# Kernel tuning notes

Measured on AMD Instinct MI355X. Metric: run time of the kernel, lower is better.

## Reference

```python
import jax, jax.numpy as jnp
import numpy as np

S, B, NC = 16, 8, 5
D, H, DH = 256, 16, 16
PS, IMG = 7, 28
P = (IMG // PS) ** 2  # 16 patches
L = 2
PD = PS * PS * 1  # 49
EF, EFT = 4, 0.5
DFT = int(EFT * D)


def layernorm(x, g, b, eps=1e-5):
    m = x.mean(-1, keepdims=True)
    v = ((x - m) ** 2).mean(-1, keepdims=True)
    return (x - m) / jnp.sqrt(v + eps) * g + b


def patchify(x):
    # 's b c (h p1) (w p2) -> s b (h w) (p1 p2 c)'
    s, bb, c, hh, ww = x.shape
    h, w = hh // PS, ww // PS
    x = x.reshape(s, bb, c, h, PS, w, PS)
    x = x.transpose(0, 1, 3, 5, 4, 6, 2)
    return x.reshape(s, bb, h * w, PS * PS * c)


def srwm(x, Wy, Wq, Wk, wb, ln_g, ln_b):
    # Stateful self-referential weight matrix layer (Irie et al. 2022).
    # x: (S, Bn, h*dh); Wy/Wq/Wk: (h, dh, dh); wb: (h, 4, dh)
    s, bn, dim = x.shape
    h, dh = Wy.shape[0], Wy.shape[1]
    xs = x.reshape(s, bn, h, dh)
    bc = lambda W: jnp.broadcast_to(W[None], (bn,) + W.shape)

    def step(carry, xt):
        Wy, Wq, Wk, wb = carry
        y = jnp.einsum('bhij,bhj->bhi', Wy, xt)
        q = jnp.einsum('bhij,bhj->bhi', Wq, xt)
        k = jnp.einsum('bhij,bhj->bhi', Wk, xt)
        beta = jax.nn.sigmoid(jnp.einsum('bhcj,bhj->bhc', wb, xt))  # (Bn,h,4)
        qs = jax.nn.softmax(q, -1)
        ks = jax.nn.softmax(k, -1)
        # old values retrieved with k, target values generated with q
        vy_k = jnp.einsum('bhij,bhj->bhi', Wy, ks)
        vq_k = jnp.einsum('bhij,bhj->bhi', Wq, ks)
        vk_k = jnp.einsum('bhij,bhj->bhi', Wk, ks)
        vb_k = jnp.einsum('bhcj,bhj->bhc', wb, ks)
        vy_q = jax.nn.softmax(jnp.einsum('bhij,bhj->bhi', Wy, qs), -1)
        vq_q = jnp.einsum('bhij,bhj->bhi', Wq, qs)
        vk_q = jnp.einsum('bhij,bhj->bhi', Wk, qs)
        vb_q = jnp.einsum('bhcj,bhj->bhc', wb, qs)
        upd = lambda d, bt: bt[..., None, None] * d[..., None] * ks[..., None, :]
        Wy = Wy + upd(vy_q - vy_k, beta[..., 0])
        Wq = Wq + upd(vq_q - vq_k, beta[..., 1])
        Wk = Wk + upd(vk_q - vk_k, beta[..., 2])
        wb = wb + beta[..., 3, None, None] * (vb_q - vb_k)[..., None] * ks[..., None, :]
        return (Wy, Wq, Wk, wb), y

    _, ys = jax.lax.scan(step, (bc(Wy), bc(Wq), bc(Wk), bc(wb)), xs)
    return layernorm(ys.reshape(s, bn, dim), ln_g, ln_b)


def setup_inputs():
    key = jax.random.key(0)
    ks = iter(jax.random.split(key, 64))
    n = lambda shape, sc: jax.random.normal(next(ks), shape, jnp.float32) * sc
    return dict(
        x=jax.random.normal(next(ks), (S, B, 1, IMG, IMG), jnp.float32),
        fb=jax.random.randint(next(ks), (S, B), 0, NC),
        in_W=n((PD + NC, D), (PD + NC) ** -0.5), in_b=jnp.zeros((D,)),
        tk_Wy=n((L, 1, P, P), P ** -0.5), tk_Wq=n((L, 1, P, P), 0.01 * P ** -0.5),
        tk_Wk=n((L, 1, P, P), P ** -0.5), tk_wb=n((L, 1, 4, P), P ** -0.5),
        tk_lng=jnp.ones((L, P)), tk_lnb=jnp.zeros((L, P)),
        tkm_g=jnp.ones((L, D)), tkm_b=jnp.zeros((L, D)),
        tkm_W1=n((L, P, EF * P), P ** -0.5), tkm_b1=jnp.zeros((L, EF * P)),
        tkm_W2=n((L, EF * P, P), (EF * P) ** -0.5), tkm_b2=jnp.zeros((L, P)),
        ch_Wy=n((L, H, DH, DH), DH ** -0.5), ch_Wq=n((L, H, DH, DH), 0.01 * DH ** -0.5),
        ch_Wk=n((L, H, DH, DH), DH ** -0.5), ch_wb=n((L, H, 4, DH), DH ** -0.5),
        ch_lng=jnp.ones((L, D)), ch_lnb=jnp.zeros((L, D)),
        chm_g=jnp.ones((L, D)), chm_b=jnp.zeros((L, D)),
        chm_W1=n((L, D, DFT), D ** -0.5), chm_b1=jnp.zeros((L, DFT)),
        chm_W2=n((L, DFT, D), DFT ** -0.5), chm_b2=jnp.zeros((L, D)),
        fln_g=jnp.ones((D,)), fln_b=jnp.zeros((D,)),
        o_Wy=n((H, DH, DH), DH ** -0.5), o_Wq=n((H, DH, DH), 0.01 * DH ** -0.5),
        o_Wk=n((H, DH, DH), DH ** -0.5), o_wb=n((H, 4, DH), DH ** -0.5),
        o_lng=jnp.ones((D,)), o_lnb=jnp.zeros((D,)),
        out_W=n((D, NC), D ** -0.5), out_b=jnp.zeros((NC,)),
    )


def reference(x, fb, in_W, in_b, tk_Wy, tk_Wq, tk_Wk, tk_wb, tk_lng, tk_lnb,
              tkm_g, tkm_b, tkm_W1, tkm_b1, tkm_W2, tkm_b2,
              ch_Wy, ch_Wq, ch_Wk, ch_wb, ch_lng, ch_lnb,
              chm_g, chm_b, chm_W1, chm_b1, chm_W2, chm_b2,
              fln_g, fln_b, o_Wy, o_Wq, o_Wk, o_wb, o_lng, o_lnb, out_W, out_b):
    xp = patchify(x)  # (S,B,P,PD)
    emb = jnp.broadcast_to(jax.nn.one_hot(fb, NC)[:, :, None, :], (S, B, P, NC))
    h = jnp.concatenate([xp, emb.astype(xp.dtype)], -1) @ in_W + in_b  # (S,B,P,D)
    for i in range(L):
        # token SRWM: features = patch axis, batch = B*D
        t = jnp.swapaxes(h, -2, -1).reshape(S, B * D, P)
        t = srwm(t, tk_Wy[i], tk_Wq[i], tk_Wk[i], tk_wb[i], tk_lng[i], tk_lnb[i])
        h = jnp.swapaxes(t.reshape(S, B, D, P), -2, -1)
        # token mixer (pre-norm residual, FFN over patch axis)
        hn = jnp.swapaxes(layernorm(h, tkm_g[i], tkm_b[i]), -2, -1)
        hn = jax.nn.gelu(hn @ tkm_W1[i] + tkm_b1[i]) @ tkm_W2[i] + tkm_b2[i]
        h = h + jnp.swapaxes(hn, -2, -1)
        # channel SRWM: features = hidden axis, batch = B*P
        c = srwm(h.reshape(S, B * P, D), ch_Wy[i], ch_Wq[i], ch_Wk[i], ch_wb[i], ch_lng[i], ch_lnb[i])
        h = c.reshape(S, B, P, D)
        # channel mixer
        hn = layernorm(h, chm_g[i], chm_b[i])
        h = h + (jax.nn.gelu(hn @ chm_W1[i] + chm_b1[i]) @ chm_W2[i] + chm_b2[i])
    h = layernorm(h, fln_g, fln_b).mean(-2)  # (S,B,D) mean over patches
    h = srwm(h, o_Wy, o_Wq, o_Wk, o_wb, o_lng, o_lnb)
    return h @ out_W + out_b  # (S,B,NC)
```

## Files before the change

### kernel.cpp

```cpp
#include <hip/hip_runtime.h>
#include <math.h>

constexpr int cS  = 16;
constexpr int cB  = 8;
constexpr int cNC = 5;
constexpr int cD  = 256;
constexpr int cP  = 16;
constexpr int cPD = 49;
#define LEPS 1e-5f

__device__ __forceinline__ float frcp(float x) { return __builtin_amdgcn_rcpf(x); }
__device__ __forceinline__ float sigm(float x) { return frcp(1.0f + __expf(-x)); }
__device__ __forceinline__ float gelu_t(float x) {
  const float z = 1.5957691216057308f * (x + 0.044715f * x * x * x);
  return x * frcp(1.0f + __expf(-z));
}

template<int CTRL>
__device__ __forceinline__ float dpp_mov(float v) {
  return __int_as_float(__builtin_amdgcn_update_dpp(
      0, __float_as_int(v), CTRL, 0xF, 0xF, true));
}
__device__ __forceinline__ float row_sum16(float v) {
  v += dpp_mov<0xB1>(v);
  v += dpp_mov<0x4E>(v);
  v += dpp_mov<0x124>(v);
  v += dpp_mov<0x128>(v);
  return v;
}
__device__ __forceinline__ float wave_sum64(float v) {
  v = row_sum16(v);
  v += __shfl_xor(v, 16, 64);
  v += __shfl_xor(v, 32, 64);
  return v;
}

__global__ __launch_bounds__(256) void k_embed(const float* __restrict__ x,
                                               const int* __restrict__ fb,
                                               const float* __restrict__ inW,
                                               const float* __restrict__ inb,
                                               float* __restrict__ h) {
  const int blk = blockIdx.x;
  const int p  = blk & 15;
  const int sb = blk >> 4;
  const int ph = p >> 2, pw = p & 3;
  __shared__ float sx[cPD];
  const int t = threadIdx.x;
  if (t < cPD) {
    const int p1 = t / 7, p2 = t % 7;
    sx[t] = x[(size_t)sb * 784 + (ph * 7 + p1) * 28 + (pw * 7 + p2)];
  }
  __syncthreads();
  const int cls = fb[sb];
  float acc = inb[t] + inW[(size_t)(cPD + cls) * cD + t];
#pragma unroll
  for (int j = 0; j < cPD; ++j) acc += sx[j] * inW[(size_t)j * cD + t];
  h[((size_t)sb * cP + p) * cD + t] = acc;
}

__global__ __launch_bounds__(256) void k_tok_srwm(
    float* __restrict__ h, const float* __restrict__ Wy0, const float* __restrict__ Wq0,
    const float* __restrict__ Wk0, const float* __restrict__ wb0,
    const float* __restrict__ lng, const float* __restrict__ lnb) {
  const int t    = threadIdx.x;
  const int lane = t & 63;
  const int w    = t >> 6;
  const int r    = lane & 15;
  const int li   = lane >> 4;
  const int b    = blockIdx.x >> 4;
  const int d    = ((blockIdx.x & 15) << 4) + (w << 2) + li;
  float wy[16], wq[16], wk[16], wbr[16];
#pragma unroll
  for (int j = 0; j < 16; ++j) {
    wy[j]  = Wy0[r * 16 + j];
    wq[j]  = Wq0[r * 16 + j];
    wk[j]  = Wk0[r * 16 + j];
    wbr[j] = wb0[(r & 3) * 16 + j];
  }
  const float gg = lng[r], bb = lnb[r];
  float xp[16];
#pragma unroll
  for (int s = 0; s < 16; ++s)
    xp[s] = h[((size_t)(s * cB + b) * cP + r) * cD + d];
  for (int s = 0; s < cS; ++s) {
    const float xv = xp[s];
    float y = 0.f, q = 0.f, k = 0.f, bt = 0.f;
#pragma unroll
    for (int j = 0; j < 16; ++j) {
      const float xj = __shfl(xv, j, 16);
      y += wy[j] * xj; q += wq[j] * xj; k += wk[j] * xj; bt += wbr[j] * xj;
    }
    const float bsig = sigm(bt);
    const float eq = __expf(q), ek = __expf(k);
    float ay = 0.f, vyk = 0.f, vqq = 0.f, vqk = 0.f, vkq = 0.f, vkk = 0.f, vbq = 0.f, vbk = 0.f;
    float ksj[16];
#pragma unroll
    for (int j = 0; j < 16; ++j) {
      const float qj = __shfl(eq, j, 16);
      const float kj = __shfl(ek, j, 16);
      ksj[j] = kj;
      ay  += wy[j]  * qj; vyk += wy[j]  * kj;
      vqq += wq[j]  * qj; vqk += wq[j]  * kj;
      vkq += wk[j]  * qj; vkk += wk[j]  * kj;
      vbq += wbr[j] * qj; vbk += wbr[j] * kj;
    }
    const float rq = frcp(row_sum16(eq));
    const float rk = frcp(row_sum16(ek));
    const float ea = __expf(ay * rq);
    const float vyq = ea * frcp(row_sum16(ea));
    const float b0  = __shfl(bsig, 0, 16);
    const float b1v = __shfl(bsig, 1, 16);
    const float b2v = __shfl(bsig, 2, 16);
    const float b3v = __shfl(bsig, 3, 16);
    const float cy = b0  * (vyq      - vyk * rk) * rk;
    const float cq = b1v * (vqq * rq - vqk * rk) * rk;
    const float ck = b2v * (vkq * rq - vkk * rk) * rk;
    const float cb = b3v * (vbq * rq - vbk * rk) * rk;
#pragma unroll
    for (int j = 0; j < 16; ++j) {
      wy[j] += cy * ksj[j]; wq[j] += cq * ksj[j]; wk[j] += ck * ksj[j]; wbr[j] += cb * ksj[j];
    }
    const float s1 = row_sum16(y);
    const float s2 = row_sum16(y * y);
    const float m = s1 * 0.0625f;
    const float var = s2 * 0.0625f - m * m;
    h[((size_t)(s * cB + b) * cP + r) * cD + d] = (y - m) * rsqrtf(var + LEPS) * gg + bb;
  }
}

__global__ __launch_bounds__(256) void k_tok_mixer(
    float* __restrict__ h, const float* __restrict__ g, const float* __restrict__ bta,
    const float* __restrict__ W1, const float* __restrict__ b1,
    const float* __restrict__ W2, const float* __restrict__ b2) {
  const int sb = blockIdx.x;
  const int t = threadIdx.x;
  __shared__ float tile[16][256];
  __shared__ float W1s[16 * 64], W2s[64 * 16];
  __shared__ float mean_[16], rstd_[16];
  __shared__ float red[16][17], red2[16][17];
  const size_t base = (size_t)sb * cP * cD;
#pragma unroll
  for (int p = 0; p < 16; ++p) tile[p][t] = h[base + p * 256 + t];
  W1s[t] = W1[t]; W1s[t + 256] = W1[t + 256]; W1s[t + 512] = W1[t + 512]; W1s[t + 768] = W1[t + 768];
  W2s[t] = W2[t]; W2s[t + 256] = W2[t + 256]; W2s[t + 512] = W2[t + 512]; W2s[t + 768] = W2[t + 768];
  __syncthreads();
  const int p = t >> 4, l = t & 15;
  float ps = 0.f, ps2 = 0.f;
#pragma unroll
  for (int k = 0; k < 16; ++k) { const float v = tile[p][l + 16 * k]; ps += v; ps2 += v * v; }
  red[p][l] = ps; red2[p][l] = ps2;
  __syncthreads();
  if (t < 16) {
    float sm = 0.f, s2 = 0.f;
#pragma unroll
    for (int k = 0; k < 16; ++k) { sm += red[t][k]; s2 += red2[t][k]; }
    const float m = sm * (1.f / 256.f);
    mean_[t] = m;
    rstd_[t] = rsqrtf(s2 * (1.f / 256.f) - m * m + LEPS);
  }
  __syncthreads();
  const float gd = g[t], bd = bta[t];
  float v[16], out[16];
#pragma unroll
  for (int pp = 0; pp < 16; ++pp) {
    v[pp] = (tile[pp][t] - mean_[pp]) * rstd_[pp] * gd + bd;
    out[pp] = b2[pp];
  }
  for (int e = 0; e < 64; ++e) {
    float acc = b1[e];
#pragma unroll
    for (int pp = 0; pp < 16; ++pp) acc += v[pp] * W1s[pp * 64 + e];
    const float ge = gelu_t(acc);
#pragma unroll
    for (int pp = 0; pp < 16; ++pp) out[pp] += ge * W2s[e * 16 + pp];
  }
#pragma unroll
  for (int pp = 0; pp < 16; ++pp) h[base + pp * 256 + t] = tile[pp][t] + out[pp];
}

__global__ __launch_bounds__(256, 1) void k_ch_srwm_mix(
    float* __restrict__ h, const float* __restrict__ Wy0, const float* __restrict__ Wq0,
    const float* __restrict__ Wk0, const float* __restrict__ wb0,
    const float* __restrict__ lng, const float* __restrict__ lnb,
    const float* __restrict__ mg, const float* __restrict__ mb,
    const float* __restrict__ W1, const float* __restrict__ b1,
    const float* __restrict__ W2, const float* __restrict__ b2) {
  const int t = threadIdx.x;
  const int hh = t >> 4, r = t & 15;
  const int bp = blockIdx.x;
  __shared__ float yout[16][256];
  __shared__ float lnv[8][256];
  __shared__ float hid[8][128];
  {
    float wy[16], wq[16], wk[16], wbr[16];
#pragma unroll
    for (int j = 0; j < 16; ++j) {
      wy[j]  = Wy0[(hh * 16 + r) * 16 + j];
      wq[j]  = Wq0[(hh * 16 + r) * 16 + j];
      wk[j]  = Wk0[(hh * 16 + r) * 16 + j];
      wbr[j] = wb0[(hh * 4 + (r & 3)) * 16 + j];
    }
    float xp[16];
#pragma unroll
    for (int s = 0; s < 16; ++s)
      xp[s] = h[(size_t)(s * cB * cP + bp) * cD + t];
    for (int s = 0; s < cS; ++s) {
      const float xv = xp[s];
      float y = 0.f, q = 0.f, k = 0.f, bt = 0.f;
#pragma unroll
      for (int j = 0; j < 16; ++j) {
        const float xj = __shfl(xv, j, 16);
        y += wy[j] * xj; q += wq[j] * xj; k += wk[j] * xj; bt += wbr[j] * xj;
      }
      yout[s][t] = y;
      const float bsig = sigm(bt);
      const float eq = __expf(q), ek = __expf(k);
      float ay = 0.f, vyk = 0.f, vqq = 0.f, vqk = 0.f, vkq = 0.f, vkk = 0.f, vbq = 0.f, vbk = 0.f;
      float ksj[16];
#pragma unroll
      for (int j = 0; j < 16; ++j) {
        const float qj = __shfl(eq, j, 16);
        const float kj = __shfl(ek, j, 16);
        ksj[j] = kj;
        ay  += wy[j]  * qj; vyk += wy[j]  * kj;
        vqq += wq[j]  * qj; vqk += wq[j]  * kj;
        vkq += wk[j]  * qj; vkk += wk[j]  * kj;
        vbq += wbr[j] * qj; vbk += wbr[j] * kj;
      }
      const float rq = frcp(row_sum16(eq));
      const float rk = frcp(row_sum16(ek));
      const float ea = __expf(ay * rq);
      const float vyq = ea * frcp(row_sum16(ea));
      const float b0  = __shfl(bsig, 0, 16);
      const float b1v = __shfl(bsig, 1, 16);
      const float b2v = __shfl(bsig, 2, 16);
      const float b3v = __shfl(bsig, 3, 16);
      const float cy = b0  * (vyq      - vyk * rk) * rk;
      const float cq = b1v * (vqq * rq - vqk * rk) * rk;
      const float ck = b2v * (vkq * rq - vkk * rk) * rk;
      const float cb = b3v * (vbq * rq - vbk * rk) * rk;
#pragma unroll
      for (int j = 0; j < 16; ++j) {
        wy[j] += cy * ksj[j]; wq[j] += cq * ksj[j]; wk[j] += ck * ksj[j]; wbr[j] += cb * ksj[j];
      }
    }
  }
  __syncthreads();
  {
    const int r32 = t >> 5, l = t & 31;
    const float4 eg0 = ((const float4*)lng)[l * 2];
    const float4 eg1 = ((const float4*)lng)[l * 2 + 1];
    const float4 eb0 = ((const float4*)lnb)[l * 2];
    const float4 eb1 = ((const float4*)lnb)[l * 2 + 1];
    const float4 mg0 = ((const float4*)mg)[l * 2];
    const float4 mg1 = ((const float4*)mg)[l * 2 + 1];
    const float4 mb0 = ((const float4*)mb)[l * 2];
    const float4 mb1 = ((const float4*)mb)[l * 2 + 1];
    for (int grp = 0; grp < 2; ++grp) {
      const int srow = grp * 8 + r32;
      const float4 y0 = ((const float4*)yout[srow])[l * 2];
      const float4 y1 = ((const float4*)yout[srow])[l * 2 + 1];
      float s1 = y0.x + y0.y + y0.z + y0.w + y1.x + y1.y + y1.z + y1.w;
      float s2 = y0.x * y0.x + y0.y * y0.y + y0.z * y0.z + y0.w * y0.w +
                 y1.x * y1.x + y1.y * y1.y + y1.z * y1.z + y1.w * y1.w;
#pragma unroll
      for (int o = 1; o < 32; o <<= 1) {
        s1 += __shfl_xor(s1, o, 32);
        s2 += __shfl_xor(s2, o, 32);
      }
      const float m1 = s1 * (1.f / 256.f);
      const float rst1 = rsqrtf(s2 * (1.f / 256.f) - m1 * m1 + LEPS);
      float4 a0, a1;
      a0.x = (y0.x - m1) * rst1 * eg0.x + eb0.x; a0.y = (y0.y - m1) * rst1 * eg0.y + eb0.y;
      a0.z = (y0.z - m1) * rst1 * eg0.z + eb0.z; a0.w = (y0.w - m1) * rst1 * eg0.w + eb0.w;
      a1.x = (y1.x - m1) * rst1 * eg1.x + eb1.x; a1.y = (y1.y - m1) * rst1 * eg1.y + eb1.y;
      a1.z = (y1.z - m1) * rst1 * eg1.z + eb1.z; a1.w = (y1.w - m1) * rst1 * eg1.w + eb1.w;
      float u1 = a0.x + a0.y + a0.z + a0.w + a1.x + a1.y + a1.z + a1.w;
      float u2 = a0.x * a0.x + a0.y * a0.y + a0.z * a0.z + a0.w * a0.w +
                 a1.x * a1.x + a1.y * a1.y + a1.z * a1.z + a1.w * a1.w;
#pragma unroll
      for (int o = 1; o < 32; o <<= 1) {
        u1 += __shfl_xor(u1, o, 32);
        u2 += __shfl_xor(u2, o, 32);
      }
      const float m2 = u1 * (1.f / 256.f);
      const float rst2 = rsqrtf(u2 * (1.f / 256.f) - m2 * m2 + LEPS);
      float4 L0, L1;
      L0.x = (a0.x - m2) * rst2 * mg0.x + mb0.x; L0.y = (a0.y - m2) * rst2 * mg0.y + mb0.y;
      L0.z = (a0.z - m2) * rst2 * mg0.z + mb0.z; L0.w = (a0.w - m2) * rst2 * mg0.w + mb0.w;
      L1.x = (a1.x - m2) * rst2 * mg1.x + mb1.x; L1.y = (a1.y - m2) * rst2 * mg1.y + mb1.y;
      L1.z = (a1.z - m2) * rst2 * mg1.z + mb1.z; L1.w = (a1.w - m2) * rst2 * mg1.w + mb1.w;
      ((float4*)lnv[r32])[l * 2]     = L0;
      ((float4*)lnv[r32])[l * 2 + 1] = L1;
      __syncthreads();
      {
        const float4* W1f = (const float4*)W1;
        float4 acc = ((const float4*)b1)[l];
        for (int j = 0; j < 256; ++j) {
          const float xj = lnv[r32][j];
          const float4 wv = W1f[j * 32 + l];
          acc.x += xj * wv.x; acc.y += xj * wv.y; acc.z += xj * wv.z; acc.w += xj * wv.w;
        }
        float4 hv;
        hv.x = gelu_t(acc.x); hv.y = gelu_t(acc.y);
        hv.z = gelu_t(acc.z); hv.w = gelu_t(acc.w);
        ((float4*)hid[r32])[l] = hv;
      }
      __syncthreads();
      {
        const float4* W2f = (const float4*)W2;
        float4 o0 = ((const float4*)b2)[l * 2];
        float4 o1 = ((const float4*)b2)[l * 2 + 1];
        for (int e = 0; e < 128; ++e) {
          const float xh = hid[r32][e];
          const float4 w0 = W2f[e * 64 + l * 2];
          const float4 w1 = W2f[e * 64 + l * 2 + 1];
          o0.x += xh * w0.x; o0.y += xh * w0.y; o0.z += xh * w0.z; o0.w += xh * w0.w;
          o1.x += xh * w1.x; o1.y += xh * w1.y; o1.z += xh * w1.z; o1.w += xh * w1.w;
        }
        o0.x += a0.x; o0.y += a0.y; o0.z += a0.z; o0.w += a0.w;
        o1.x += a1.x; o1.y += a1.y; o1.z += a1.z; o1.w += a1.w;
        float4* op = (float4*)(h + (size_t)(srow * cB * cP + bp) * cD);
        op[l * 2]     = o0;
        op[l * 2 + 1] = o1;
      }
      __syncthreads();
    }
  }
}

__global__ __launch_bounds__(256) void k_fln_mean(
    const float* __restrict__ h, const float* __restrict__ gg, const float* __restrict__ bbv,
    float* __restrict__ o) {
  const int sb = blockIdx.x;
  const int t = threadIdx.x;
  const int lane = t & 63, w = t >> 6;
  const float4 g4 = ((const float4*)gg)[lane];
  const float4 b4 = ((const float4*)bbv)[lane];
  float a0 = 0.f, a1 = 0.f, a2 = 0.f, a3 = 0.f;
  for (int pp = 0; pp < 4; ++pp) {
    const int p = w * 4 + pp;
    const float4 v4 = ((const float4*)(h + ((size_t)sb * cP + p) * cD))[lane];
    const float s1 = wave_sum64(v4.x + v4.y + v4.z + v4.w);
    const float s2 = wave_sum64(v4.x * v4.x + v4.y * v4.y + v4.z * v4.z + v4.w * v4.w);
    const float m = s1 * (1.f / 256.f);
    const float rst = rsqrtf(s2 * (1.f / 256.f) - m * m + LEPS);
    a0 += (v4.x - m) * rst * g4.x + b4.x;
    a1 += (v4.y - m) * rst * g4.y + b4.y;
    a2 += (v4.z - m) * rst * g4.z + b4.z;
    a3 += (v4.w - m) * rst * g4.w + b4.w;
  }
  __shared__ float sacc[4][256];
  float4* sp = (float4*)sacc[w];
  sp[lane] = make_float4(a0, a1, a2, a3);
  __syncthreads();
  o[(size_t)sb * cD + t] = (sacc[0][t] + sacc[1][t] + sacc[2][t] + sacc[3][t]) * (1.f / 16.f);
}

__global__ __launch_bounds__(256, 1) void k_out_srwm(
    const float* __restrict__ gin, float* __restrict__ outp,
    const float* __restrict__ Wy0, const float* __restrict__ Wq0,
    const float* __restrict__ Wk0, const float* __restrict__ wb0,
    const float* __restrict__ lng, const float* __restrict__ lnb,
    const float* __restrict__ outW, const float* __restrict__ outb) {
  const int t = threadIdx.x;
  const int lane = t & 63;
  const int w = t >> 6;
  const int hh = t >> 4, r = t & 15;
  const int b = blockIdx.x;
  __shared__ float ymat[16][256];
  __shared__ float gwm[cNC][256];
  __shared__ float GBp[4][10];
  __shared__ float GBs[10];
  float wy[16], wq[16], wk[16], wbr[16];
#pragma unroll
  for (int j = 0; j < 16; ++j) {
    wy[j]  = Wy0[(hh * 16 + r) * 16 + j];
    wq[j]  = Wq0[(hh * 16 + r) * 16 + j];
    wk[j]  = Wk0[(hh * 16 + r) * 16 + j];
    wbr[j] = wb0[(hh * 4 + (r & 3)) * 16 + j];
  }
  {
    const float gg = lng[t], bbl = lnb[t];
    float pg[cNC], pbv[cNC];
#pragma unroll
    for (int c = 0; c < cNC; ++c) {
      const float wv = outW[(size_t)t * cNC + c];
      const float gwv = gg * wv;
      gwm[c][t] = gwv;
      pg[c] = wave_sum64(gwv);
      pbv[c] = wave_sum64(bbl * wv);
    }
    if (lane == 0) {
#pragma unroll
      for (int c = 0; c < cNC; ++c) { GBp[w][c] = pg[c]; GBp[w][5 + c] = pbv[c]; }
    }
    __syncthreads();
    if (t < 10) GBs[t] = GBp[0][t] + GBp[1][t] + GBp[2][t] + GBp[3][t];
    __syncthreads();
  }
  float xp[16];
#pragma unroll
  for (int s = 0; s < 16; ++s) xp[s] = gin[(size_t)(s * cB + b) * cD + t];
  for (int s = 0; s < cS; ++s) {
    const float xv = xp[s];
    float y = 0.f, q = 0.f, k = 0.f, bt = 0.f;
#pragma unroll
    for (int j = 0; j < 16; ++j) {
      const float xj = __shfl(xv, j, 16);
      y += wy[j] * xj; q += wq[j] * xj; k += wk[j] * xj; bt += wbr[j] * xj;
    }
    ymat[s][t] = y;
    const float bsig = sigm(bt);
    const float eq = __expf(q), ek = __expf(k);
    float ay = 0.f, vyk = 0.f, vqq = 0.f, vqk = 0.f, vkq = 0.f, vkk = 0.f, vbq = 0.f, vbk = 0.f;
    float ksj[16];
#pragma unroll
    for (int j = 0; j < 16; ++j) {
      const float qj = __shfl(eq, j, 16);
      const float kj = __shfl(ek, j, 16);
      ksj[j] = kj;
      ay  += wy[j]  * qj; vyk += wy[j]  * kj;
      vqq += wq[j]  * qj; vqk += wq[j]  * kj;
      vkq += wk[j]  * qj; vkk += wk[j]  * kj;
      vbq += wbr[j] * qj; vbk += wbr[j] * kj;
    }
    const float rq = frcp(row_sum16(eq));
    const float rk = frcp(row_sum16(ek));
    const float ea = __expf(ay * rq);
    const float vyq = ea * frcp(row_sum16(ea));
    const float b0  = __shfl(bsig, 0, 16);
    const float b1v = __shfl(bsig, 1, 16);
    const float b2v = __shfl(bsig, 2, 16);
    const float b3v = __shfl(bsig, 3, 16);
    const float cy = b0  * (vyq      - vyk * rk) * rk;
    const float cq = b1v * (vqq * rq - vqk * rk) * rk;
    const float ck = b2v * (vkq * rq - vkk * rk) * rk;
    const float cb = b3v * (vbq * rq - vbk * rk) * rk;
#pragma unroll
    for (int j = 0; j < 16; ++j) {
      wy[j] += cy * ksj[j]; wq[j] += cq * ksj[j]; wk[j] += ck * ksj[j]; wbr[j] += cb * ksj[j];
    }
  }
  __syncthreads();
  for (int k2 = 0; k2 < 4; ++k2) {
    const int sidx = w * 4 + k2;
    const float4 y4 = ((const float4*)ymat[sidx])[lane];
    const float s1 = wave_sum64(y4.x + y4.y + y4.z + y4.w);
    const float s2 = wave_sum64(y4.x * y4.x + y4.y * y4.y + y4.z * y4.z + y4.w * y4.w);
    float S[cNC];
#pragma unroll
    for (int c = 0; c < cNC; ++c) {
      const float4 g4 = ((const float4*)gwm[c])[lane];
      S[c] = wave_sum64(y4.x * g4.x + y4.y * g4.y + y4.z * g4.z + y4.w * g4.w);
    }
    if (lane == 0) {
      const float m = s1 * (1.f / 256.f);
      const float var = s2 * (1.f / 256.f) - m * m;
      const float rst = rsqrtf(var + LEPS);
#pragma unroll
      for (int c = 0; c < cNC; ++c) {
        outp[(size_t)(sidx * cB + b) * cNC + c] =
            outb[c] + rst * S[c] - rst * m * GBs[c] + GBs[5 + c];
      }
    }
  }
}

extern "C" void kernel_launch(void* const* d_in, const int* in_sizes, int n_in,
                              void* d_out, int out_size, void* d_ws, size_t ws_size,
                              hipStream_t stream) {
  const float* x     = (const float*)d_in[0];
  const int*   fb    = (const int*)d_in[1];
  const float* inW   = (const float*)d_in[2];
  const float* inb   = (const float*)d_in[3];
  const float* tkWy  = (const float*)d_in[4];
  const float* tkWq  = (const float*)d_in[5];
  const float* tkWk  = (const float*)d_in[6];
  const float* tkwb  = (const float*)d_in[7];
  const float* tklng = (const float*)d_in[8];
  const float* tklnb = (const float*)d_in[9];
  const float* tkmg  = (const float*)d_in[10];
  const float* tkmb  = (const float*)d_in[11];
  const float* tkmW1 = (const float*)d_in[12];
  const float* tkmb1 = (const float*)d_in[13];
  const float* tkmW2 = (const float*)d_in[14];
  const float* tkmb2 = (const float*)d_in[15];
  const float* chWy  = (const float*)d_in[16];
  const float* chWq  = (const float*)d_in[17];
  const float* chWk  = (const float*)d_in[18];
  const float* chwb  = (const float*)d_in[19];
  const float* chlng = (const float*)d_in[20];
  const float* chlnb = (const float*)d_in[21];
  const float* chmg  = (const float*)d_in[22];
  const float* chmb  = (const float*)d_in[23];
  const float* chmW1 = (const float*)d_in[24];
  const float* chmb1 = (const float*)d_in[25];
  const float* chmW2 = (const float*)d_in[26];
  const float* chmb2 = (const float*)d_in[27];
  const float* flng  = (const float*)d_in[28];
  const float* flnb  = (const float*)d_in[29];
  const float* oWy   = (const float*)d_in[30];
  const float* oWq   = (const float*)d_in[31];
  const float* oWk   = (const float*)d_in[32];
  const float* owb   = (const float*)d_in[33];
  const float* olng  = (const float*)d_in[34];
  const float* olnb  = (const float*)d_in[35];
  const float* outW  = (const float*)d_in[36];
  const float* outb  = (const float*)d_in[37];

  float* h    = (float*)d_ws;
  float* gbuf = h + (size_t)cS * cB * cP * cD;
  float* outp = (float*)d_out;

  k_embed<<<dim3(cS * cB * cP), dim3(256), 0, stream>>>(x, fb, inW, inb, h);
  for (int i = 0; i < 2; ++i) {
    k_tok_srwm<<<dim3(128), dim3(256), 0, stream>>>(
        h, tkWy + i * 256, tkWq + i * 256, tkWk + i * 256, tkwb + i * 64,
        tklng + i * 16, tklnb + i * 16);
    k_tok_mixer<<<dim3(cS * cB), dim3(256), 0, stream>>>(
        h, tkmg + i * 256, tkmb + i * 256, tkmW1 + i * 1024, tkmb1 + i * 64,
        tkmW2 + i * 1024, tkmb2 + i * 16);
    k_ch_srwm_mix<<<dim3(cB * cP), dim3(256), 0, stream>>>(
        h, chWy + i * 4096, chWq + i * 4096, chWk + i * 4096, chwb + i * 1024,
        chlng + i * 256, chlnb + i * 256,
        chmg + i * 256, chmb + i * 256, chmW1 + i * 32768, chmb1 + i * 128,
        chmW2 + i * 32768, chmb2 + i * 256);
  }
  k_fln_mean<<<dim3(cS * cB), dim3(256), 0, stream>>>(h, flng, flnb, gbuf);
  k_out_srwm<<<dim3(cB), dim3(256), 0, stream>>>(
      gbuf, outp, oWy, oWq, oWk, owb, olng, olnb, outW, outb);
}
```

Measured before the change: 334.0 us.

## Split channel SRWM scan from LN+mixer and widen grids for more parallelism

The fused channel SRWM+mixer kernel, which ran on only 128 blocks with a serial 16-step mixer, is split in two. A scan kernel runs on 256 blocks of 128 threads, one per head-group, and writes y to a workspace buffer. A separate LN+MLP kernel runs on 256 blocks, each handling 8 rows. The token SRWM is relaunched as 256 blocks of 128 threads, and the shared scan step moves into a helper function. This trades an extra global round-trip of y and one more launch for much better GPU occupancy.

Result: faster. 313.9 us, median of 2 (-6.0%).

```diff
diff --git a/kernel.cpp b/kernel.cpp
--- a/kernel.cpp
+++ b/kernel.cpp
@@ -33,6 +33,47 @@
   v += __shfl_xor(v, 16, 64);
   v += __shfl_xor(v, 32, 64);
   return v;
+}
+
+__device__ __forceinline__ float srwm_step(
+    float xv, float (&wy)[16], float (&wq)[16], float (&wk)[16], float (&wbr)[16]) {
+  float y = 0.f, q = 0.f, k = 0.f, bt = 0.f;
+#pragma unroll
+  for (int j = 0; j < 16; ++j) {
+    const float xj = __shfl(xv, j, 16);
+    y += wy[j] * xj; q += wq[j] * xj; k += wk[j] * xj; bt += wbr[j] * xj;
+  }
+  const float bsig = sigm(bt);
+  const float eq = __expf(q), ek = __expf(k);
+  float ay = 0.f, vyk = 0.f, vqq = 0.f, vqk = 0.f, vkq = 0.f, vkk = 0.f, vbq = 0.f, vbk = 0.f;
+  float ksj[16];
+#pragma unroll
+  for (int j = 0; j < 16; ++j) {
+    const float qj = __shfl(eq, j, 16);
+    const float kj = __shfl(ek, j, 16);
+    ksj[j] = kj;
+    ay  += wy[j]  * qj; vyk += wy[j]  * kj;
+    vqq += wq[j]  * qj; vqk += wq[j]  * kj;
+    vkq += wk[j]  * qj; vkk += wk[j]  * kj;
+    vbq += wbr[j] * qj; vbk += wbr[j] * kj;
+  }
+  const float rq = frcp(row_sum16(eq));
+  const float rk = frcp(row_sum16(ek));
+  const float ea = __expf(ay * rq);
+  const float vyq = ea * frcp(row_sum16(ea));
+  const float b0  = __shfl(bsig, 0, 16);
+  const float b1v = __shfl(bsig, 1, 16);
+  const float b2v = __shfl(bsig, 2, 16);
+  const float b3v = __shfl(bsig, 3, 16);
+  const float cy = b0  * (vyq      - vyk * rk) * rk;
+  const float cq = b1v * (vqq * rq - vqk * rk) * rk;
+  const float ck = b2v * (vkq * rq - vkk * rk) * rk;
+  const float cb = b3v * (vbq * rq - vbk * rk) * rk;
+#pragma unroll
+  for (int j = 0; j < 16; ++j) {
+    wy[j] += cy * ksj[j]; wq[j] += cq * ksj[j]; wk[j] += ck * ksj[j]; wbr[j] += cb * ksj[j];
+  }
+  return y;
 }
 
 __global__ __launch_bounds__(256) void k_embed(const float* __restrict__ x,
@@ -58,7 +99,7 @@
   h[((size_t)sb * cP + p) * cD + t] = acc;
 }
 
-__global__ __launch_bounds__(256) void k_tok_srwm(
+__global__ __launch_bounds__(128) void k_tok_srwm(
     float* __restrict__ h, const float* __restrict__ Wy0, const float* __restrict__ Wq0,
     const float* __restrict__ Wk0, const float* __restrict__ wb0,
     const float* __restrict__ lng, const float* __restrict__ lnb) {
@@ -67,8 +108,8 @@
   const int w    = t >> 6;
   const int r    = lane & 15;
   const int li   = lane >> 4;
-  const int b    = blockIdx.x >> 4;
-  const int d    = ((blockIdx.x & 15) << 4) + (w << 2) + li;
+  const int b    = blockIdx.x >> 5;
+  const int d    = ((blockIdx.x & 31) << 3) + (w << 2) + li;
   float wy[16], wq[16], wk[16], wbr[16];
 #pragma unroll
   for (int j = 0; j < 16; ++j) {
@@ -83,43 +124,7 @@
   for (int s = 0; s < 16; ++s)
     xp[s] = h[((size_t)(s * cB + b) * cP + r) * cD + d];
   for (int s = 0; s < cS; ++s) {
-    const float xv = xp[s];
-    float y = 0.f, q = 0.f, k = 0.f, bt = 0.f;
-#pragma unroll
-    for (int j = 0; j < 16; ++j) {
-      const float xj = __shfl(xv, j, 16);
-      y += wy[j] * xj; q += wq[j] * xj; k += wk[j] * xj; bt += wbr[j] * xj;
-    }
-    const float bsig = sigm(bt);
-    const float eq = __expf(q), ek = __expf(k);
-    float ay = 0.f, vyk = 0.f, vqq = 0.f, vqk = 0.f, vkq = 0.f, vkk = 0.f, vbq = 0.f, vbk = 0.f;
-    float ksj[16];
-#pragma unroll
-    for (int j = 0; j < 16; ++j) {
-      const float qj = __shfl(eq, j, 16);
-      const float kj = __shfl(ek, j, 16);
-      ksj[j] = kj;
-      ay  += wy[j]  * qj; vyk += wy[j]  * kj;
-      vqq += wq[j]  * qj; vqk += wq[j]  * kj;
-      vkq += wk[j]  * qj; vkk += wk[j]  * kj;
-      vbq += wbr[j] * qj; vbk += wbr[j] * kj;
-    }
-    const float rq = frcp(row_sum16(eq));
-    const float rk = frcp(row_sum16(ek));
-    const float ea = __expf(ay * rq);
-    const float vyq = ea * frcp(row_sum16(ea));
-    const float b0  = __shfl(bsig, 0, 16);
-    const float b1v = __shfl(bsig, 1, 16);
-    const float b2v = __shfl(bsig, 2, 16);
-    const float b3v = __shfl(bsig, 3, 16);
-    const float cy = b0  * (vyq      - vyk * rk) * rk;
-    const float cq = b1v * (vqq * rq - vqk * rk) * rk;
-    const float ck = b2v * (vkq * rq - vkk * rk) * rk;
-    const float cb = b3v * (vbq * rq - vbk * rk) * rk;
-#pragma unroll
-    for (int j = 0; j < 16; ++j) {
-      wy[j] += cy * ksj[j]; wq[j] += cq * ksj[j]; wk[j] += ck * ksj[j]; wbr[j] += cb * ksj[j];
-    }
+    const float y = srwm_step(xp[s], wy, wq, wk, wbr);
     const float s1 = row_sum16(y);
     const float s2 = row_sum16(y * y);
     const float m = s1 * 0.0625f;
@@ -178,154 +183,121 @@
   for (int pp = 0; pp < 16; ++pp) h[base + pp * 256 + t] = tile[pp][t] + out[pp];
 }
 
-__global__ __launch_bounds__(256, 1) void k_ch_srwm_mix(
-    float* __restrict__ h, const float* __restrict__ Wy0, const float* __restrict__ Wq0,
-    const float* __restrict__ Wk0, const float* __restrict__ wb0,
+__global__ __launch_bounds__(128) void k_ch_scan(
+    const float* __restrict__ h, float* __restrict__ y2,
+    const float* __restrict__ Wy0, const float* __restrict__ Wq0,
+    const float* __restrict__ Wk0, const float* __restrict__ wb0) {
+  const int t  = threadIdx.x;
+  const int hg = blockIdx.x & 1;
+  const int bp = blockIdx.x >> 1;
+  const int hh = (hg << 3) + (t >> 4);
+  const int r  = t & 15;
+  const int d  = (hg << 7) + t;
+  float wy[16], wq[16], wk[16], wbr[16];
+#pragma unroll
+  for (int j = 0; j < 16; ++j) {
+    wy[j]  = Wy0[(hh * 16 + r) * 16 + j];
+    wq[j]  = Wq0[(hh * 16 + r) * 16 + j];
+    wk[j]  = Wk0[(hh * 16 + r) * 16 + j];
+    wbr[j] = wb0[(hh * 4 + (r & 3)) * 16 + j];
+  }
+  float xp[16];
+#pragma unroll
+  for (int s = 0; s < 16; ++s)
+    xp[s] = h[(size_t)(s * cB * cP + bp) * cD + d];
+  for (int s = 0; s < cS; ++s)
+    y2[(size_t)(s * cB * cP + bp) * cD + d] = srwm_step(xp[s], wy, wq, wk, wbr);
+}
+
+__global__ __launch_bounds__(256) void k_ch_ln_mix(
+    const float* __restrict__ y2, float* __restrict__ h,
     const float* __restrict__ lng, const float* __restrict__ lnb,
     const float* __restrict__ mg, const float* __restrict__ mb,
     const float* __restrict__ W1, const float* __restrict__ b1,
     const float* __restrict__ W2, const float* __restrict__ b2) {
   const int t = threadIdx.x;
-  const int hh = t >> 4, r = t & 15;
-  const int bp = blockIdx.x;
-  __shared__ float yout[16][256];
+  const int row0 = blockIdx.x * 8;
+  __shared__ float yv[8][256];
   __shared__ float lnv[8][256];
   __shared__ float hid[8][128];
+  const float4* yp4 = (const float4*)(y2 + (size_t)row0 * cD);
+  ((float4*)yv)[t]       = yp4[t];
+  ((float4*)yv)[t + 256] = yp4[t + 256];
+  __syncthreads();
+  const int r32 = t >> 5, l = t & 31;
+  const float4 eg0 = ((const float4*)lng)[l * 2];
+  const float4 eg1 = ((const float4*)lng)[l * 2 + 1];
+  const float4 eb0 = ((const float4*)lnb)[l * 2];
+  const float4 eb1 = ((const float4*)lnb)[l * 2 + 1];
+  const float4 mg0 = ((const float4*)mg)[l * 2];
+  const float4 mg1 = ((const float4*)mg)[l * 2 + 1];
+  const float4 mb0 = ((const float4*)mb)[l * 2];
+  const float4 mb1 = ((const float4*)mb)[l * 2 + 1];
+  const float4 y0 = ((const float4*)yv[r32])[l * 2];
+  const float4 y1 = ((const float4*)yv[r32])[l * 2 + 1];
+  float s1 = y0.x + y0.y + y0.z + y0.w + y1.x + y1.y + y1.z + y1.w;
+  float s2 = y0.x * y0.x + y0.y * y0.y + y0.z * y0.z + y0.w * y0.w +
+             y1.x * y1.x + y1.y * y1.y + y1.z * y1.z + y1.w * y1.w;
+#pragma unroll
+  for (int o = 1; o < 32; o <<= 1) {
+    s1 += __shfl_xor(s1, o, 32);
+    s2 += __shfl_xor(s2, o, 32);
+  }
+  const float m1 = s1 * (1.f / 256.f);
+  const float rst1 = rsqrtf(s2 * (1.f / 256.f) - m1 * m1 + LEPS);
+  float4 a0, a1;
+  a0.x = (y0.x - m1) * rst1 * eg0.x + eb0.x; a0.y = (y0.y - m1) * rst1 * eg0.y + eb0.y;
+  a0.z = (y0.z - m1) * rst1 * eg0.z + eb0.z; a0.w = (y0.w - m1) * rst1 * eg0.w + eb0.w;
+  a1.x = (y1.x - m1) * rst1 * eg1.x + eb1.x; a1.y = (y1.y - m1) * rst1 * eg1.y + eb1.y;
+  a1.z = (y1.z - m1) * rst1 * eg1.z + eb1.z; a1.w = (y1.w - m1) * rst1 * eg1.w + eb1.w;
+  float u1 = a0.x + a0.y + a0.z + a0.w + a1.x + a1.y + a1.z + a1.w;
+  float u2 = a0.x * a0.x + a0.y * a0.y + a0.z * a0.z + a0.w * a0.w +
+             a1.x * a1.x + a1.y * a1.y + a1.z * a1.z + a1.w * a1.w;
+#pragma unroll
+  for (int o = 1; o < 32; o <<= 1) {
+    u1 += __shfl_xor(u1, o, 32);
+    u2 += __shfl_xor(u2, o, 32);
+  }
+  const float m2 = u1 * (1.f / 256.f);
+  const float rst2 = rsqrtf(u2 * (1.f / 256.f) - m2 * m2 + LEPS);
+  float4 L0, L1;
+  L0.x = (a0.x - m2) * rst2 * mg0.x + mb0.x; L0.y = (a0.y - m2) * rst2 * mg0.y + mb0.y;
+  L0.z = (a0.z - m2) * rst2 * mg0.z + mb0.z; L0.w = (a0.w - m2) * rst2 * mg0.w + mb0.w;
+  L1.x = (a1.x - m2) * rst2 * mg1.x + mb1.x; L1.y = (a1.y - m2) * rst2 * mg1.y + mb1.y;
+  L1.z = (a1.z - m2) * rst2 * mg1.z + mb1.z; L1.w = (a1.w - m2) * rst2 * mg1.w + mb1.w;
+  ((float4*)lnv[r32])[l * 2]     = L0;
+  ((float4*)lnv[r32])[l * 2 + 1] = L1;
+  __syncthreads();
   {
-    float wy[16], wq[16], wk[16], wbr[16];
-#pragma unroll
-    for (int j = 0; j < 16; ++j) {
-      wy[j]  = Wy0[(hh * 16 + r) * 16 + j];
-      wq[j]  = Wq0[(hh * 16 + r) * 16 + j];
-      wk[j]  = Wk0[(hh * 16 + r) * 16 + j];
-      wbr[j] = wb0[(hh * 4 + (r & 3)) * 16 + j];
-    }
-    float xp[16];
-#pragma unroll
-    for (int s = 0; s < 16; ++s)
-      xp[s] = h[(size_t)(s * cB * cP + bp) * cD + t];
-    for (int s = 0; s < cS; ++s) {
-      const float xv = xp[s];
-      float y = 0.f, q = 0.f, k = 0.f, bt = 0.f;
-#pragma unroll
-      for (int j = 0; j < 16; ++j) {
-        const float xj = __shfl(xv, j, 16);
-        y += wy[j] * xj; q += wq[j] * xj; k += wk[j] * xj; bt += wbr[j] * xj;
-      }
-      yout[s][t] = y;
-      const float bsig = sigm(bt);
-      const float eq = __expf(q), ek = __expf(k);
-      float ay = 0.f, vyk = 0.f, vqq = 0.f, vqk = 0.f, vkq = 0.f, vkk = 0.f, vbq = 0.f, vbk = 0.f;
-      float ksj[16];
-#pragma unroll
-      for (int j = 0; j < 16; ++j) {
-        const float qj = __shfl(eq, j, 16);
-        const float kj = __shfl(ek, j, 16);
-        ksj[j] = kj;
-        ay  += wy[j]  * qj; vyk += wy[j]  * kj;
-        vqq += wq[j]  * qj; vqk += wq[j]  * kj;
-        vkq += wk[j]  * qj; vkk += wk[j]  * kj;
-        vbq += wbr[j] * qj; vbk += wbr[j] * kj;
-      }
-      const float rq = frcp(row_sum16(eq));
-      const float rk = frcp(row_sum16(ek));
-      const float ea = __expf(ay * rq);
-      const float vyq = ea * frcp(row_sum16(ea));
-      const float b0  = __shfl(bsig, 0, 16);
-      const float b1v = __shfl(bsig, 1, 16);
-      const float b2v = __shfl(bsig, 2, 16);
-      const float b3v = __shfl(bsig, 3, 16);
-      const float cy = b0  * (vyq      - vyk * rk) * rk;
-      const float cq = b1v * (vqq * rq - vqk * rk) * rk;
-      const float ck = b2v * (vkq * rq - vkk * rk) * rk;
-      const float cb = b3v * (vbq * rq - vbk * rk) * rk;
-#pragma unroll
-      for (int j = 0; j < 16; ++j) {
-        wy[j] += cy * ksj[j]; wq[j] += cq * ksj[j]; wk[j] += ck * ksj[j]; wbr[j] += cb * ksj[j];
-      }
-    }
+    const float4* W1f = (const float4*)W1;
+    float4 acc = ((const float4*)b1)[l];
+    for (int j = 0; j < 256; ++j) {
+      const float xj = lnv[r32][j];
+      const float4 wv = W1f[j * 32 + l];
+      acc.x += xj * wv.x; acc.y += xj * wv.y; acc.z += xj * wv.z; acc.w += xj * wv.w;
+    }
+    float4 hv;
+    hv.x = gelu_t(acc.x); hv.y = gelu_t(acc.y);
+    hv.z = gelu_t(acc.z); hv.w = gelu_t(acc.w);
+    ((float4*)hid[r32])[l] = hv;
   }
   __syncthreads();
   {
-    const int r32 = t >> 5, l = t & 31;
-    const float4 eg0 = ((const float4*)lng)[l * 2];
-    const float4 eg1 = ((const float4*)lng)[l * 2 + 1];
-    const float4 eb0 = ((const float4*)lnb)[l * 2];
-    const float4 eb1 = ((const float4*)lnb)[l * 2 + 1];
-    const float4 mg0 = ((const float4*)mg)[l * 2];
-    const float4 mg1 = ((const float4*)mg)[l * 2 + 1];
-    const float4 mb0 = ((const float4*)mb)[l * 2];
-    const float4 mb1 = ((const float4*)mb)[l * 2 + 1];
-    for (int grp = 0; grp < 2; ++grp) {
-      const int srow = grp * 8 + r32;
-      const float4 y0 = ((const float4*)yout[srow])[l * 2];
-      const float4 y1 = ((const float4*)yout[srow])[l * 2 + 1];
-      float s1 = y0.x + y0.y + y0.z + y0.w + y1.x + y1.y + y1.z + y1.w;
-      float s2 = y0.x * y0.x + y0.y * y0.y + y0.z * y0.z + y0.w * y0.w +
-                 y1.x * y1.x + y1.y * y1.y + y1.z * y1.z + y1.w * y1.w;
-#pragma unroll
-      for (int o = 1; o < 32; o <<= 1) {
-        s1 += __shfl_xor(s1, o, 32);
-        s2 += __shfl_xor(s2, o, 32);
-      }
-      const float m1 = s1 * (1.f / 256.f);
-      const float rst1 = rsqrtf(s2 * (1.f / 256.f) - m1 * m1 + LEPS);
-      float4 a0, a1;
-      a0.x = (y0.x - m1) * rst1 * eg0.x + eb0.x; a0.y = (y0.y - m1) * rst1 * eg0.y + eb0.y;
-      a0.z = (y0.z - m1) * rst1 * eg0.z + eb0.z; a0.w = (y0.w - m1) * rst1 * eg0.w + eb0.w;
-      a1.x = (y1.x - m1) * rst1 * eg1.x + eb1.x; a1.y = (y1.y - m1) * rst1 * eg1.y + eb1.y;
-      a1.z = (y1.z - m1) * rst1 * eg1.z + eb1.z; a1.w = (y1.w - m1) * rst1 * eg1.w + eb1.w;
-      float u1 = a0.x + a0.y + a0.z + a0.w + a1.x + a1.y + a1.z + a1.w;
-      float u2 = a0.x * a0.x + a0.y * a0.y + a0.z * a0.z + a0.w * a0.w +
-                 a1.x * a1.x + a1.y * a1.y + a1.z * a1.z + a1.w * a1.w;
-#pragma unroll
-      for (int o = 1; o < 32; o <<= 1) {
-        u1 += __shfl_xor(u1, o, 32);
-        u2 += __shfl_xor(u2, o, 32);
-      }
-      const float m2 = u1 * (1.f / 256.f);
-      const float rst2 = rsqrtf(u2 * (1.f / 256.f) - m2 * m2 + LEPS);
-      float4 L0, L1;
-      L0.x = (a0.x - m2) * rst2 * mg0.x + mb0.x; L0.y = (a0.y - m2) * rst2 * mg0.y + mb0.y;
-      L0.z = (a0.z - m2) * rst2 * mg0.z + mb0.z; L0.w = (a0.w - m2) * rst2 * mg0.w + mb0.w;
-      L1.x = (a1.x - m2) * rst2 * mg1.x + mb1.x; L1.y = (a1.y - m2) * rst2 * mg1.y + mb1.y;
-      L1.z = (a1.z - m2) * rst2 * mg1.z + mb1.z; L1.w = (a1.w - m2) * rst2 * mg1.w + mb1.w;
-      ((float4*)lnv[r32])[l * 2]     = L0;
-      ((float4*)lnv[r32])[l * 2 + 1] = L1;
-      __syncthreads();
-      {
-        const float4* W1f = (const float4*)W1;
-        float4 acc = ((const float4*)b1)[l];
-        for (int j = 0; j < 256; ++j) {
-          const float xj = lnv[r32][j];
-          const float4 wv = W1f[j * 32 + l];
-          acc.x += xj * wv.x; acc.y += xj * wv.y; acc.z += xj * wv.z; acc.w += xj * wv.w;
-        }
-        float4 hv;
-        hv.x = gelu_t(acc.x); hv.y = gelu_t(acc.y);
-        hv.z = gelu_t(acc.z); hv.w = gelu_t(acc.w);
-        ((float4*)hid[r32])[l] = hv;
-      }
-      __syncthreads();
-      {
-        const float4* W2f = (const float4*)W2;
-        float4 o0 = ((const float4*)b2)[l * 2];
-        float4 o1 = ((const float4*)b2)[l * 2 + 1];
-        for (int e = 0; e < 128; ++e) {
-          const float xh = hid[r32][e];
-          const float4 w0 = W2f[e * 64 + l * 2];
-          const float4 w1 = W2f[e * 64 + l * 2 + 1];
-          o0.x += xh * w0.x; o0.y += xh * w0.y; o0.z += xh * w0.z; o0.w += xh * w0.w;
-          o1.x += xh * w1.x; o1.y += xh * w1.y; o1.z += xh * w1.z; o1.w += xh * w1.w;
-        }
-        o0.x += a0.x; o0.y += a0.y; o0.z += a0.z; o0.w += a0.w;
-        o1.x += a1.x; o1.y += a1.y; o1.z += a1.z; o1.w += a1.w;
-        float4* op = (float4*)(h + (size_t)(srow * cB * cP + bp) * cD);
-        op[l * 2]     = o0;
-        op[l * 2 + 1] = o1;
-      }
-      __syncthreads();
-    }
+    const float4* W2f = (const float4*)W2;
+    float4 o0 = ((const float4*)b2)[l * 2];
+    float4 o1 = ((const float4*)b2)[l * 2 + 1];
+    for (int e = 0; e < 128; ++e) {
+      const float xh = hid[r32][e];
+      const float4 w0 = W2f[e * 64 + l * 2];
+      const float4 w1 = W2f[e * 64 + l * 2 + 1];
+      o0.x += xh * w0.x; o0.y += xh * w0.y; o0.z += xh * w0.z; o0.w += xh * w0.w;
+      o1.x += xh * w1.x; o1.y += xh * w1.y; o1.z += xh * w1.z; o1.w += xh * w1.w;
+    }
+    o0.x += a0.x; o0.y += a0.y; o0.z += a0.z; o0.w += a0.w;
+    o1.x += a1.x; o1.y += a1.y; o1.z += a1.z; o1.w += a1.w;
+    float4* op = (float4*)(h + ((size_t)row0 + r32) * cD);
+    op[l * 2]     = o0;
+    op[l * 2 + 1] = o1;
   }
 }
 
@@ -402,46 +374,8 @@
   float xp[16];
 #pragma unroll
   for (int s = 0; s < 16; ++s) xp[s] = gin[(size_t)(s * cB + b) * cD + t];
-  for (int s = 0; s < cS; ++s) {
-    const float xv = xp[s];
-    float y = 0.f, q = 0.f, k = 0.f, bt = 0.f;
-#pragma unroll
-    for (int j = 0; j < 16; ++j) {
-      const float xj = __shfl(xv, j, 16);
-      y += wy[j] * xj; q += wq[j] * xj; k += wk[j] * xj; bt += wbr[j] * xj;
-    }
-    ymat[s][t] = y;
-    const float bsig = sigm(bt);
-    const float eq = __expf(q), ek = __expf(k);
-    float ay = 0.f, vyk = 0.f, vqq = 0.f, vqk = 0.f, vkq = 0.f, vkk = 0.f, vbq = 0.f, vbk = 0.f;
-    float ksj[16];
-#pragma unroll
-    for (int j = 0; j < 16; ++j) {
-      const float qj = __shfl(eq, j, 16);
-      const float kj = __shfl(ek, j, 16);
-      ksj[j] = kj;
-      ay  += wy[j]  * qj; vyk += wy[j]  * kj;
-      vqq += wq[j]  * qj; vqk += wq[j]  * kj;
-      vkq += wk[j]  * qj; vkk += wk[j]  * kj;
-      vbq += wbr[j] * qj; vbk += wbr[j] * kj;
-    }
-    const float rq = frcp(row_sum16(eq));
-    const float rk = frcp(row_sum16(ek));
-    const float ea = __expf(ay * rq);
-    const float vyq = ea * frcp(row_sum16(ea));
-    const float b0  = __shfl(bsig, 0, 16);
-    const float b1v = __shfl(bsig, 1, 16);
-    const float b2v = __shfl(bsig, 2, 16);
-    const float b3v = __shfl(bsig, 3, 16);
-    const float cy = b0  * (vyq      - vyk * rk) * rk;
-    const float cq = b1v * (vqq * rq - vqk * rk) * rk;
-    const float ck = b2v * (vkq * rq - vkk * rk) * rk;
-    const float cb = b3v * (vbq * rq - vbk * rk) * rk;
-#pragma unroll
-    for (int j = 0; j < 16; ++j) {
-      wy[j] += cy * ksj[j]; wq[j] += cq * ksj[j]; wk[j] += ck * ksj[j]; wbr[j] += cb * ksj[j];
-    }
-  }
+  for (int s = 0; s < cS; ++s)
+    ymat[s][t] = srwm_step(xp[s], wy, wq, wk, wbr);
   __syncthreads();
   for (int k2 = 0; k2 < 4; ++k2) {
     const int sidx = w * 4 + k2;
@@ -511,19 +445,21 @@
 
   float* h    = (float*)d_ws;
   float* gbuf = h + (size_t)cS * cB * cP * cD;
+  float* y2   = gbuf + (size_t)cS * cB * cD;
   float* outp = (float*)d_out;
 
   k_embed<<<dim3(cS * cB * cP), dim3(256), 0, stream>>>(x, fb, inW, inb, h);
   for (int i = 0; i < 2; ++i) {
-    k_tok_srwm<<<dim3(128), dim3(256), 0, stream>>>(
+    k_tok_srwm<<<dim3(256), dim3(128), 0, stream>>>(
         h, tkWy + i * 256, tkWq + i * 256, tkWk + i * 256, tkwb + i * 64,
         tklng + i * 16, tklnb + i * 16);
     k_tok_mixer<<<dim3(cS * cB), dim3(256), 0, stream>>>(
         h, tkmg + i * 256, tkmb + i * 256, tkmW1 + i * 1024, tkmb1 + i * 64,
         tkmW2 + i * 1024, tkmb2 + i * 16);
-    k_ch_srwm_mix<<<dim3(cB * cP), dim3(256), 0, stream>>>(
-        h, chWy + i * 4096, chWq + i * 4096, chWk + i * 4096, chwb + i * 1024,
-        chlng + i * 256, chlnb + i * 256,
+    k_ch_scan<<<dim3(cB * cP * 2), dim3(128), 0, stream>>>(
+        h, y2, chWy + i * 4096, chWq + i * 4096, chWk + i * 4096, chwb + i * 1024);
+    k_ch_ln_mix<<<dim3(cS * cB * cP / 8), dim3(256), 0, stream>>>(
+        y2, h, chlng + i * 256, chlnb + i * 256,
         chmg + i * 256, chmb + i * 256, chmW1 + i * 32768, chmb1 + i * 128,
         chmW2 + i * 32768, chmb2 + i * 256);
   }
```
